# Optimization experiments

Measured on AMD Instinct MI355X. Metric: run time of the kernel, lower is better.

Reference implementation:

```python
import jax, jax.numpy as jnp
import numpy as np

PRE_NMS_TOPK = 6000
POST_NMS_TOPK = 1000
NMS_THRESH = 0.7
MIN_SIZE = 16.0
NEG = -1e9  # stand-in for -inf that is safe under autodiff


def setup_inputs() -> dict:
    key = jax.random.key(0)
    k1, k2, k3, k4, k5, k6, k7, k8 = jax.random.split(key, 8)
    B, A = 8, 200000
    N = B * A
    # realistic anchors: centers within a ~1333x800 canvas, sizes 16..256
    cx = jax.random.uniform(k1, (N,), minval=0.0, maxval=1200.0)
    cy = jax.random.uniform(k2, (N,), minval=0.0, maxval=800.0)
    w = jax.random.uniform(k3, (N,), minval=16.0, maxval=256.0)
    h = jax.random.uniform(k4, (N,), minval=16.0, maxval=256.0)
    anchors = jnp.stack([cx - 0.5 * w, cy - 0.5 * h, cx + 0.5 * w, cy + 0.5 * h], axis=1)
    batch_indices = jnp.sort(jax.random.randint(k5, (N,), 0, B)).astype(jnp.int32)
    image_sizes = jax.random.randint(k6, (B, 2), 600, 1334).astype(jnp.int32)  # (H, W)
    objectness_logits = jax.random.normal(k7, (N, 1), dtype=jnp.float32)
    bbox_deltas = jax.random.normal(k8, (N, 4), dtype=jnp.float32) * 0.2
    return {
        'anchors': anchors,
        'batch_indices': batch_indices,
        'image_sizes': image_sizes,
        'objectness_logits': objectness_logits,
        'bbox_deltas': bbox_deltas,
    }


def _nms_one(bx, sc):
    """Greedy NMS on [K,4] boxes / [K] scores; returns POST_NMS_TOPK (idx, ok)."""
    K = bx.shape[0]
    areas = (bx[:, 2] - bx[:, 0]) * (bx[:, 3] - bx[:, 1])
    ar = jnp.arange(K)

    def step(sup, _):
        s = jnp.where(sup, NEG, sc)
        j = jnp.argmax(s)
        ok = s[j] > 0.5 * NEG
        b = bx[j]
        ix1 = jnp.maximum(b[0], bx[:, 0])
        iy1 = jnp.maximum(b[1], bx[:, 1])
        ix2 = jnp.minimum(b[2], bx[:, 2])
        iy2 = jnp.minimum(b[3], bx[:, 3])
        inter = jnp.maximum(ix2 - ix1, 0.0) * jnp.maximum(iy2 - iy1, 0.0)
        iou = inter / (areas + areas[j] - inter + 1e-9)
        sup = sup | (iou > NMS_THRESH) | (ar == j)
        return sup, (j, ok)

    sup0 = sc <= 0.5 * NEG  # padded / invalid entries start suppressed
    _, (idx, ok) = jax.lax.scan(step, sup0, None, length=POST_NMS_TOPK)
    return idx, ok


def reference(anchors, batch_indices, image_sizes, objectness_logits, bbox_deltas):
    B = image_sizes.shape[0]
    N = anchors.shape[0]
    sizes = image_sizes[batch_indices].astype(jnp.float32)  # [N,2] (H,W) per anchor

    # --- box decode ---
    a_w = anchors[:, 2] - anchors[:, 0]
    a_h = anchors[:, 3] - anchors[:, 1]
    a_x = anchors[:, 0] + 0.5 * a_w
    a_y = anchors[:, 1] + 0.5 * a_h
    t_x, t_y = bbox_deltas[:, 0], bbox_deltas[:, 1]
    t_w, t_h = bbox_deltas[:, 2], bbox_deltas[:, 3]
    p_x = a_x + t_x * a_w
    p_y = a_y + t_y * a_h
    p_w = a_w * jnp.exp(jnp.clip(t_w, -10.0, 10.0))
    p_h = a_h * jnp.exp(jnp.clip(t_h, -10.0, 10.0))
    x1 = p_x - 0.5 * p_w
    y1 = p_y - 0.5 * p_h
    x2 = p_x + 0.5 * p_w
    y2 = p_y + 0.5 * p_h

    # --- clip to image ---
    H, W = sizes[:, 0], sizes[:, 1]
    x1 = jnp.clip(x1, 0.0, W - 1.0)
    y1 = jnp.clip(y1, 0.0, H - 1.0)
    x2 = jnp.clip(x2, 0.0, W - 1.0)
    y2 = jnp.clip(y2, 0.0, H - 1.0)
    boxes = jnp.stack([x1, y1, x2, y2], axis=1)  # [N,4]

    # --- min-size filter (as score masking) ---
    valid = ((x2 - x1) >= MIN_SIZE) & ((y2 - y1) >= MIN_SIZE)
    fg = jax.nn.sigmoid(objectness_logits[:, 0])

    # --- per-image top-k over masked scores ---
    img_mask = batch_indices[None, :] == jnp.arange(B, dtype=batch_indices.dtype)[:, None]  # [B,N]
    scores = jnp.where(img_mask & valid[None, :], fg[None, :], NEG)  # [B,N]
    top_scores, top_idx = jax.lax.top_k(scores, PRE_NMS_TOPK)  # [B,PRE]
    top_boxes = boxes[top_idx]  # [B,PRE,4]

    # --- NMS per image ---
    keep_idx, keep_ok = jax.vmap(_nms_one)(top_boxes, top_scores)  # [B,POST]

    sel = jnp.take_along_axis(top_idx, keep_idx, axis=1)  # global anchor indices [B,POST]
    okf = keep_ok[..., None].astype(boxes.dtype)
    props = jnp.take_along_axis(top_boxes, keep_idx[..., None], axis=1) * okf  # [B,POST,4]
    obj = objectness_logits[sel] * okf  # [B,POST,1]
    deltas_out = bbox_deltas[sel] * okf  # [B,POST,4]
    bidx = jnp.where(keep_ok, jnp.arange(B, dtype=jnp.int32)[:, None], -1)  # [B,POST]

    return (props.reshape(-1, 4), bidx.reshape(-1), obj.reshape(-1, 1),
            deltas_out.reshape(-1, 4), keep_ok.reshape(-1))
```

## Files before the change

### kernel.cpp

```cpp
#include <hip/hip_runtime.h>
#include <stdint.h>

#define PRE_K   6000
#define POST_K  1000
#define CAP     8192
#define BINS    1024
#define ROWS    6016
#define CH      94
#define MASKW   188
#define RC_CH   32
#define ROW_CAP (RC_CH * 64)
#define NEGF    -1000000000.0f
#define IOU_EPS 16.0f


__device__ __forceinline__ uint32_t orderf(float f) {
  uint32_t u = __float_as_uint(f);
  return (u & 0x80000000u) ? ~u : (u | 0x80000000u);
}

__device__ __forceinline__ int score_bin(float sc) {
  int bin = (int)floorf((sc + 12.0f) * ((float)BINS / 24.0f));
  return bin < 0 ? 0 : (bin > BINS - 1 ? BINS - 1 : bin);
}

__device__ __forceinline__ int bin_slot(int bin) {
  return ((bin & 15) << 6) | (bin >> 4);
}

__device__ __forceinline__ void decode_box(
    const float* __restrict__ anchors, const float* __restrict__ deltas,
    const int* __restrict__ isz, int n, int b,
    double& x1, double& y1, double& x2, double& y2, bool& valid) {
  double ax1 = (double)anchors[4 * n + 0], ay1 = (double)anchors[4 * n + 1];
  double ax2 = (double)anchors[4 * n + 2], ay2 = (double)anchors[4 * n + 3];
  double aw = ax2 - ax1, ah = ay2 - ay1;
  double acx = ax1 + 0.5 * aw, acy = ay1 + 0.5 * ah;
  double tx = (double)deltas[4 * n + 0], ty = (double)deltas[4 * n + 1];
  double tw = (double)deltas[4 * n + 2], th = (double)deltas[4 * n + 3];
  tw = tw < -10.0 ? -10.0 : (tw > 10.0 ? 10.0 : tw);
  th = th < -10.0 ? -10.0 : (th > 10.0 ? 10.0 : th);
  double px = acx + tx * aw, py = acy + ty * ah;
  double pw = aw * exp(tw), ph = ah * exp(th);
  double H = (double)isz[2 * b + 0], W = (double)isz[2 * b + 1];
  double wm = W - 1.0, hm = H - 1.0;
  x1 = px - 0.5 * pw; y1 = py - 0.5 * ph;
  x2 = px + 0.5 * pw; y2 = py + 0.5 * ph;
  x1 = fmin(fmax(x1, 0.0), wm); x2 = fmin(fmax(x2, 0.0), wm);
  y1 = fmin(fmax(y1, 0.0), hm); y2 = fmin(fmax(y2, 0.0), hm);
  valid = (x2 - x1 >= 16.0) && (y2 - y1 >= 16.0);
}

__device__ __forceinline__ bool iou_exact(const double* __restrict__ tbox,
                                          const double* __restrict__ tarea,
                                          size_t ri, size_t ci) {
  const double* pr = &tbox[ri * 4];
  const double* pc = &tbox[ci * 4];
  double w = fmin(pr[2], pc[2]) - fmax(pr[0], pc[0]); w = w > 0.0 ? w : 0.0;
  double h = fmin(pr[3], pc[3]) - fmax(pr[1], pc[1]); h = h > 0.0 ? h : 0.0;
  double it = w * h;
  return it > 0.7 * (tarea[ri] + tarea[ci] - it + 1e-9);
}


__global__ void k_init(uint32_t* hist, uint32_t* cnt, int B) {
  int i = blockIdx.x * blockDim.x + threadIdx.x;
  if (i < B * BINS) hist[i] = 0u;
  if (i < B) cnt[i] = 0u;
}

__global__ void __launch_bounds__(256) k_score(const float* __restrict__ anchors,
                                               const int* __restrict__ bix,
                                               const int* __restrict__ isz,
                                               const float* __restrict__ logits,
                                               const float* __restrict__ deltas,
                                               float* __restrict__ scores,
                                               uint32_t* __restrict__ hist, int N) {
  const int SPAN = 4096;
  int start = blockIdx.x * SPAN;
  int end = start + SPAN < N ? start + SPAN : N;
  __shared__ uint32_t lh[2][BINS];
  for (int i = threadIdx.x; i < 2 * BINS; i += 256) ((uint32_t*)lh)[i] = 0u;
  __shared__ int s_b0, s_b1;
  if (threadIdx.x == 0) { s_b0 = bix[start]; s_b1 = bix[end - 1]; }
  __syncthreads();
  int b0 = s_b0, b1 = s_b1;

  for (int n = start + (int)threadIdx.x; n < end; n += 256) {
    int b = bix[n];
    double x1, y1, x2, y2; bool valid;
    decode_box(anchors, deltas, isz, n, b, x1, y1, x2, y2, valid);
    float sc = valid ? logits[n] : NEGF;
    scores[n] = sc;
    if (valid) {
      int bin = score_bin(sc);
      if (b == b0)      atomicAdd(&lh[0][bin], 1u);
      else if (b == b1) atomicAdd(&lh[1][bin], 1u);
      else              atomicAdd(&hist[b * BINS + bin_slot(bin)], 1u);
    }
  }
  __syncthreads();
  for (int bin = threadIdx.x; bin < BINS; bin += 256) {
    uint32_t c0 = lh[0][bin];
    if (c0) atomicAdd(&hist[b0 * BINS + bin_slot(bin)], c0);
    if (b1 != b0) {
      uint32_t c1 = lh[1][bin];
      if (c1) atomicAdd(&hist[b1 * BINS + bin_slot(bin)], c1);
    }
  }
}

__global__ void k_scan(const uint32_t* __restrict__ hist, uint32_t* __restrict__ bstar) {
  __shared__ uint32_t s[BINS];
  __shared__ int bs;
  int b = blockIdx.x, t = threadIdx.x;
  s[t] = hist[b * BINS + bin_slot(t)];
  if (t == 0) bs = 0;
  __syncthreads();
  for (int off = 1; off < BINS; off <<= 1) {
    uint32_t v = (t + off < BINS) ? s[t + off] : 0u;
    __syncthreads();
    s[t] += v;
    __syncthreads();
  }
  if (s[t] >= PRE_K) atomicMax(&bs, t);
  __syncthreads();
  if (t == 0) bstar[b] = (uint32_t)bs;
}

__global__ void __launch_bounds__(1024) k_compact(const float* __restrict__ scores,
                                                  const int* __restrict__ bix,
                                                  const uint32_t* __restrict__ bstar,
                                                  uint32_t* __restrict__ cnt,
                                                  uint64_t* __restrict__ cand, int N) {
  const int SPAN = 8192;
  int start = blockIdx.x * SPAN;
  int end = start + SPAN < N ? start + SPAN : N;
  __shared__ uint32_t lcnt[8], lbase[8];
  if (threadIdx.x < 8) lcnt[threadIdx.x] = 0u;
  __syncthreads();

  bool     predv[8];
  uint64_t keyv[8];
  uint32_t lposv[8];
  int      bv[8];
  int nt = 0;
  for (int base = start; base < end; base += 1024, nt++) {
    int n = base + (int)threadIdx.x;
    bool pred = false; int b = 0; uint64_t key = 0ull; uint32_t lp = 0u;
    if (n < end) {
      float sc = scores[n];
      if (sc > 0.5f * NEGF) {
        b = bix[n];
        if ((uint32_t)score_bin(sc) >= bstar[b]) {
          pred = true;
          key = ((uint64_t)orderf(sc) << 32) | (uint64_t)(uint32_t)(~(uint32_t)n);
          lp = atomicAdd(&lcnt[b], 1u);
        }
      }
    }
    predv[nt] = pred; keyv[nt] = key; lposv[nt] = lp; bv[nt] = b;
  }
  __syncthreads();
  if (threadIdx.x < 8) {
    uint32_t c = lcnt[threadIdx.x];
    lbase[threadIdx.x] = c ? atomicAdd(&cnt[threadIdx.x], c) : 0u;
  }
  __syncthreads();
  for (int k = 0; k < nt; k++) {
    if (predv[k]) {
      uint32_t pos = lbase[bv[k]] + lposv[k];
      if (pos < CAP) cand[(size_t)bv[k] * CAP + pos] = keyv[k];
    }
  }
}

__global__ void __launch_bounds__(256) k_rank(const uint64_t* __restrict__ cand,
                                              const uint32_t* __restrict__ cnt,
                                              int* __restrict__ sorted_n,
                                              int* __restrict__ Cnum) {
  int b = blockIdx.x >> 5, chunk = blockIdx.x & 31, t = threadIdx.x;
  int C = (int)min(cnt[b], (uint32_t)CAP);
  if (chunk == 0 && t == 0) Cnum[b] = C < PRE_K ? C : PRE_K;
  if (chunk * 256 >= C) return;
  const uint64_t* g = cand + (size_t)b * CAP;
  int i = chunk * 256 + t;
  uint64_t ki = (i < C) ? g[i] : 0ull;
  __shared__ uint64_t tile[1024];
  int rank = 0;
  for (int base = 0; base < C; base += 1024) {
#pragma unroll
    for (int u = 0; u < 4; u++) {
      int j = base + u * 256 + t;
      tile[u * 256 + t] = (j < C) ? g[j] : 0ull;
    }
    __syncthreads();
    int lim = min(1024, C - base);
    int jj = 0;
    for (; jj + 4 <= lim; jj += 4) {
      rank += (tile[jj + 0] > ki) ? 1 : 0;
      rank += (tile[jj + 1] > ki) ? 1 : 0;
      rank += (tile[jj + 2] > ki) ? 1 : 0;
      rank += (tile[jj + 3] > ki) ? 1 : 0;
    }
    for (; jj < lim; jj++) rank += (tile[jj] > ki) ? 1 : 0;
    __syncthreads();
  }
  if (i < C && rank < PRE_K)
    sorted_n[b * PRE_K + rank] = (int)(~(uint32_t)(ki & 0xFFFFFFFFull));
}

__global__ void k_gather(const float* __restrict__ anchors,
                         const float* __restrict__ deltas,
                         const int* __restrict__ isz,
                         const int* __restrict__ sorted_n,
                         const int* __restrict__ Cnum,
                         double* __restrict__ tbox, double* __restrict__ tarea,
                         float4* __restrict__ tboxf, float* __restrict__ tareaf,
                         int* __restrict__ top_n, int B) {
  int idx = blockIdx.x * blockDim.x + threadIdx.x;
  if (idx >= B * PRE_K) return;
  int b = idx / PRE_K, r = idx % PRE_K;
  if (r >= Cnum[b]) return;
  int n = sorted_n[idx];
  double x1, y1, x2, y2; bool valid;
  decode_box(anchors, deltas, isz, n, b, x1, y1, x2, y2, valid);
  size_t row = (size_t)b * ROWS + r;
  tbox[row * 4 + 0] = x1;
  tbox[row * 4 + 1] = y1;
  tbox[row * 4 + 2] = x2;
  tbox[row * 4 + 3] = y2;
  double ar = (x2 - x1) * (y2 - y1);
  tarea[row] = ar;
  tboxf[row] = make_float4((float)x1, (float)y1, (float)x2, (float)y2);
  tareaf[row] = (float)ar;
  top_n[idx] = n;
}

__global__ void __launch_bounds__(64) k_iou_mat(const float4* __restrict__ tboxf,
                                                const float* __restrict__ tareaf,
                                                const double* __restrict__ tbox,
                                                const double* __restrict__ tarea,
                                                const int* __restrict__ Cnum,
                                                uint32_t* __restrict__ maskT) {
  int blk = blockIdx.x;
  int k  = blk % (RC_CH + 1);
  int cc = (blk / (RC_CH + 1)) % CH;
  int b  = blk / ((RC_CH + 1) * CH);
  int rc = (k == RC_CH) ? cc : k;
  if (k < RC_CH && cc <= rc) return;
  int C = Cnum[b];
  if (rc * 64 >= C || cc * 64 >= C) return;
  int lane = threadIdx.x;
  size_t bb = (size_t)b * ROWS;

  float4 cb4 = tboxf[bb + (size_t)cc * 64 + lane];
  float  cba = tareaf[bb + (size_t)cc * 64 + lane];
  __shared__ float4 rbx[64];
  __shared__ float  rba[64];
  rbx[lane] = tboxf[bb + (size_t)rc * 64 + lane];
  rba[lane] = tareaf[bb + (size_t)rc * 64 + lane];
  __syncthreads();

  uint32_t* seg = maskT + (((size_t)b * CH + cc) * ROWS + (size_t)rc * 64) * 2;
  bool isdiag = (rc == cc);

  for (int i = 0; i < 64; i++) {
    float4 r4 = rbx[i];
    float ra = rba[i];
    float iw = fminf(r4.z, cb4.z) - fmaxf(r4.x, cb4.x);
    float ih = fminf(r4.w, cb4.w) - fmaxf(r4.y, cb4.y);
    iw = fmaxf(iw, 0.0f); ih = fmaxf(ih, 0.0f);
    float inter = iw * ih;
    float diff = inter - 0.7f * (ra + cba - inter);
    bool gt = isdiag ? (lane > i) : true;
    unsigned long long sup   = __ballot(gt && (diff >  IOU_EPS));
    unsigned long long loose = __ballot(gt && (diff > -IOU_EPS));
    unsigned long long border = loose & ~sup;
    if (border) {
      bool mine = (border >> lane) & 1ull;
      bool ex = false;
      if (mine)
        ex = iou_exact(tbox, tarea, bb + (size_t)rc * 64 + i,
                       bb + (size_t)cc * 64 + lane);
      sup |= __ballot(ex);
    }
    if (lane == 0) {
      seg[i * 2 + 0] = (uint32_t)sup;
      seg[i * 2 + 1] = (uint32_t)(sup >> 32);
    }
  }
}

__global__ void __launch_bounds__(256) k_nms_reduce(const uint32_t* __restrict__ maskT,
                                                    const float4* __restrict__ tboxf,
                                                    const float* __restrict__ tareaf,
                                                    const double* __restrict__ tbox,
                                                    const double* __restrict__ tarea,
                                                    const int* __restrict__ Cnum,
                                                    int* __restrict__ keep,
                                                    int* __restrict__ kept_count) {
  int b = blockIdx.x, t = threadIdx.x;
  int wave = t >> 6, lane = t & 63;
  int C = Cnum[b];
  const uint32_t* M = maskT + (size_t)b * CH * ROWS * 2;
  size_t bb = (size_t)b * ROWS;

  __shared__ uint32_t s_f[2][2];
  __shared__ uint32_t kept_lo[POST_K];
  __shared__ uint32_t kept_hi[POST_K];
  __shared__ uint64_t s_kept;
  if (t < 4) ((uint32_t*)s_f)[t] = 0u;

  uint32_t d0 = 0u, d1 = 0u;
  if (wave == 0) {
    const uint32_t* rp = M + (size_t)lane * 2;
    d0 = rp[0]; d1 = rp[1];
  }
  __syncthreads();

  int nkept = 0, nlo = 0, nhi = 0;
  for (int c = 0; c < CH; c++) {
    int base = c * 64;
    if (base >= C) break;
    int cbuf = c & 1;
    if (t == 0) { s_f[cbuf ^ 1][0] = 0u; s_f[cbuf ^ 1][1] = 0u; }

    uint32_t f0 = 0u, f1 = 0u;
    for (int k2 = t; k2 < nlo; k2 += 256) {
      const uint32_t* rp = M + ((size_t)c * ROWS + kept_lo[k2]) * 2;
      f0 |= rp[0]; f1 |= rp[1];
    }
    if (wave == 1 && nhi > 0) {
      float4 cb4 = tboxf[bb + base + lane];
      float  cba = tareaf[bb + base + lane];
      for (int k2 = 0; k2 < nhi; k2++) {
        int r = (int)kept_hi[k2];
        float4 r4 = tboxf[bb + r];
        float ra = tareaf[bb + r];
        float iw = fminf(r4.z, cb4.z) - fmaxf(r4.x, cb4.x);
        float ih = fminf(r4.w, cb4.w) - fmaxf(r4.y, cb4.y);
        iw = fmaxf(iw, 0.0f); ih = fmaxf(ih, 0.0f);
        float inter = iw * ih;
        float diff = inter - 0.7f * (ra + cba - inter);
        unsigned long long sup   = __ballot(diff >  IOU_EPS);
        unsigned long long loose = __ballot(diff > -IOU_EPS);
        unsigned long long border = loose & ~sup;
        if (border) {
          bool mine = (border >> lane) & 1ull;
          bool ex = false;
          if (mine) ex = iou_exact(tbox, tarea, bb + r, bb + base + lane);
          sup |= __ballot(ex);
        }
        f0 |= (uint32_t)sup; f1 |= (uint32_t)(sup >> 32);
      }
    }
#pragma unroll
    for (int off = 32; off > 0; off >>= 1) {
      f0 |= (uint32_t)__shfl_xor((int)f0, off, 64);
      f1 |= (uint32_t)__shfl_xor((int)f1, off, 64);
    }
    if (lane == 0 && (f0 | f1)) {
      atomicOr(&s_f[cbuf][0], f0);
      atomicOr(&s_f[cbuf][1], f1);
    }
    __syncthreads();

    if (wave == 0) {
      uint64_t sup = (uint64_t)s_f[cbuf][0] | ((uint64_t)s_f[cbuf][1] << 32);
      int rem = C - base;
      if (rem < 64) sup |= ~((1ull << rem) - 1ull);
      uint64_t diag = (uint64_t)d0 | ((uint64_t)d1 << 32);
      int cn = (c + 1 < CH) ? c + 1 : c;
      const uint32_t* rpn = M + ((size_t)cn * ROWS + (size_t)cn * 64 + lane) * 2;
      uint32_t pn0 = rpn[0], pn1 = rpn[1];

      uint64_t keptMask = 0ull;
      uint64_t alive = ~sup;
      uint64_t m = alive;
      while (m) {
        int i = __builtin_ctzll(m);
        keptMask |= 1ull << i;
        uint64_t d = (uint64_t)__shfl((long long)diag, i, 64);
        sup |= d | (1ull << i);
        m = alive & ~sup;
      }
      int allowed = POST_K - nkept;
      int pc = __popcll(keptMask);
      while (pc > allowed) {
        keptMask &= ~(1ull << (63 - __builtin_clzll(keptMask)));
        pc--;
      }
      if (lane == 0) s_kept = keptMask;
      if ((keptMask >> lane) & 1ull) {
        int pfx = __popcll(keptMask & ((1ull << lane) - 1ull));
        keep[b * POST_K + nkept + pfx] = base + lane;
        if (c < RC_CH) kept_lo[nlo + pfx] = (uint32_t)(base + lane);
        else           kept_hi[nhi + pfx] = (uint32_t)(base + lane);
      }
      d0 = pn0; d1 = pn1;
    }
    __syncthreads();

    int pc = __popcll(s_kept);
    nkept += pc;
    if (c < RC_CH) nlo += pc; else nhi += pc;
    if (nkept >= POST_K) break;
  }
  if (t == 0) kept_count[b] = nkept;
}

__global__ void k_output(const int* __restrict__ keep,
                         const int* __restrict__ kept_count,
                         const int* __restrict__ top_n,
                         const double* __restrict__ tbox,
                         const float* __restrict__ logits,
                         const float* __restrict__ deltas,
                         float* __restrict__ out, int B) {
  int idx = blockIdx.x * blockDim.x + threadIdx.x;
  int M = B * POST_K;
  if (idx >= M) return;
  int b = idx / POST_K, s = idx % POST_K;
  float p0 = 0.f, p1 = 0.f, p2 = 0.f, p3 = 0.f;
  float ob = 0.f, d0 = 0.f, d1 = 0.f, d2 = 0.f, d3 = 0.f;
  float bi = -1.0f, okv = 0.0f;
  if (s < kept_count[b]) {
    int j = keep[b * POST_K + s];
    int n = top_n[b * PRE_K + j];
    const double* p = &tbox[((size_t)b * ROWS + j) * 4];
    p0 = (float)p[0]; p1 = (float)p[1]; p2 = (float)p[2]; p3 = (float)p[3];
    ob = logits[n];
    d0 = deltas[4 * n + 0]; d1 = deltas[4 * n + 1];
    d2 = deltas[4 * n + 2]; d3 = deltas[4 * n + 3];
    bi = (float)b; okv = 1.0f;
  }
  out[idx * 4 + 0] = p0;
  out[idx * 4 + 1] = p1;
  out[idx * 4 + 2] = p2;
  out[idx * 4 + 3] = p3;
  out[4 * M + idx] = bi;
  out[5 * M + idx] = ob;
  out[6 * M + idx * 4 + 0] = d0;
  out[6 * M + idx * 4 + 1] = d1;
  out[6 * M + idx * 4 + 2] = d2;
  out[6 * M + idx * 4 + 3] = d3;
  out[10 * M + idx] = okv;
}


extern "C" void kernel_launch(void* const* d_in, const int* in_sizes, int n_in,
                              void* d_out, int out_size, void* d_ws, size_t ws_size,
                              hipStream_t stream) {
  const float* anchors = (const float*)d_in[0];
  const int*   bix     = (const int*)d_in[1];
  const int*   isz     = (const int*)d_in[2];
  const float* logits  = (const float*)d_in[3];
  const float* deltas  = (const float*)d_in[4];
  float* out = (float*)d_out;

  int N = in_sizes[1];
  int B = in_sizes[2] / 2;

  uintptr_t p = (uintptr_t)d_ws;
  double*   tbox   = (double*)p;    p += (size_t)B * ROWS * 4 * sizeof(double);
  double*   tarea  = (double*)p;    p += (size_t)B * ROWS * sizeof(double);
  uint64_t* cand   = (uint64_t*)p;  p += (size_t)B * CAP * sizeof(uint64_t);
  float*    scores = (float*)p;     p += (size_t)N * sizeof(float);
  uint32_t* hist   = (uint32_t*)p;  p += (size_t)B * BINS * sizeof(uint32_t);
  int*      sorted_n = (int*)p;     p += (size_t)B * PRE_K * sizeof(int);
  int*      top_n    = (int*)p;     p += (size_t)B * PRE_K * sizeof(int);
  int*      keep     = (int*)p;     p += (size_t)B * POST_K * sizeof(int);
  uint32_t* cnt      = (uint32_t*)p; p += (size_t)B * sizeof(uint32_t);
  uint32_t* bstar    = (uint32_t*)p; p += (size_t)B * sizeof(uint32_t);
  int*      Cnum     = (int*)p;      p += (size_t)B * sizeof(int);
  int*      kept_cnt = (int*)p;      p += (size_t)B * sizeof(int);
  p = (p + 255) & ~(uintptr_t)255;
  uint32_t* maskT    = (uint32_t*)p; p += (size_t)B * CH * ROWS * 2 * sizeof(uint32_t);
  float4*   tboxf  = (float4*)scores;
  float*    tareaf = (float*)(scores + (size_t)B * ROWS * 4);
  (void)ws_size; (void)n_in; (void)out_size;

  int initN = B * BINS;
  k_init<<<(initN + 255) / 256, 256, 0, stream>>>(hist, cnt, B);
  k_score<<<(N + 4095) / 4096, 256, 0, stream>>>(anchors, bix, isz, logits, deltas,
                                                 scores, hist, N);
  k_scan<<<B, BINS, 0, stream>>>(hist, bstar);
  k_compact<<<(N + 8191) / 8192, 1024, 0, stream>>>(scores, bix, bstar, cnt, cand, N);
  k_rank<<<B * 32, 256, 0, stream>>>(cand, cnt, sorted_n, Cnum);
  k_gather<<<(B * PRE_K + 255) / 256, 256, 0, stream>>>(anchors, deltas, isz,
                                                        sorted_n, Cnum, tbox,
                                                        tarea, tboxf, tareaf,
                                                        top_n, B);
  k_iou_mat<<<B * CH * (RC_CH + 1), 64, 0, stream>>>(tboxf, tareaf, tbox, tarea,
                                                     Cnum, maskT);
  k_nms_reduce<<<B, 256, 0, stream>>>(maskT, tboxf, tareaf, tbox, tarea, Cnum,
                                      keep, kept_cnt);
  k_output<<<(B * POST_K + 255) / 256, 256, 0, stream>>>(keep, kept_cnt, top_n,
                                                         tbox, logits, deltas,
                                                         out, B);
}
```

Baseline: 441.5 us.

## Split rank counting across comparison-range blocks with atomic partial ranks

The rank-by-counting sort now divides the comparison range into four slices, each handled by its own block, which adds partial counts into a per-candidate rank buffer with atomics. A new placement kernel then scatters the candidate indices using the summed ranks. The shared-memory tile is read as 128-bit pairs. The goal is four times as many blocks for the quadratic rank step, so more of the GPU is busy. The cost is an extra kernel launch, a larger init pass and atomic traffic.

```diff
diff --git a/kernel.cpp b/kernel.cpp
--- a/kernel.cpp
+++ b/kernel.cpp
@@ -7,9 +7,8 @@
 #define BINS    1024
 #define ROWS    6016
 #define CH      94
-#define MASKW   188
 #define RC_CH   32
-#define ROW_CAP (RC_CH * 64)
+#define JSPLIT  4
 #define NEGF    -1000000000.0f
 #define IOU_EPS 16.0f
 
@@ -63,10 +62,11 @@
 }
 
 
-__global__ void k_init(uint32_t* hist, uint32_t* cnt, int B) {
+__global__ void k_init(uint32_t* hist, uint32_t* cnt, uint32_t* prank, int B) {
   int i = blockIdx.x * blockDim.x + threadIdx.x;
   if (i < B * BINS) hist[i] = 0u;
   if (i < B) cnt[i] = 0u;
+  if (i < B * CAP) prank[i] = 0u;
 }
 
 __global__ void __launch_bounds__(256) k_score(const float* __restrict__ anchors,
@@ -177,37 +177,69 @@
 
 __global__ void __launch_bounds__(256) k_rank(const uint64_t* __restrict__ cand,
                                               const uint32_t* __restrict__ cnt,
-                                              int* __restrict__ sorted_n,
-                                              int* __restrict__ Cnum) {
-  int b = blockIdx.x >> 5, chunk = blockIdx.x & 31, t = threadIdx.x;
+                                              uint32_t* __restrict__ prank) {
+  int blk = blockIdx.x;
+  int js = blk % JSPLIT;
+  int ic = (blk / JSPLIT) % 32;
+  int b  = blk / (JSPLIT * 32);
+  int t = threadIdx.x;
   int C = (int)min(cnt[b], (uint32_t)CAP);
-  if (chunk == 0 && t == 0) Cnum[b] = C < PRE_K ? C : PRE_K;
-  if (chunk * 256 >= C) return;
+  if (ic * 256 >= C) return;
   const uint64_t* g = cand + (size_t)b * CAP;
-  int i = chunk * 256 + t;
+  int i = ic * 256 + t;
   uint64_t ki = (i < C) ? g[i] : 0ull;
+
+  int q = (C + JSPLIT - 1) / JSPLIT;
+  int j0 = js * q;
+  int j1 = j0 + q < C ? j0 + q : C;
+  if (j0 >= j1) return;
+
   __shared__ uint64_t tile[1024];
   int rank = 0;
-  for (int base = 0; base < C; base += 1024) {
+  for (int base = j0; base < j1; base += 1024) {
 #pragma unroll
     for (int u = 0; u < 4; u++) {
       int j = base + u * 256 + t;
-      tile[u * 256 + t] = (j < C) ? g[j] : 0ull;
+      tile[u * 256 + t] = (j < j1) ? g[j] : 0ull;
     }
     __syncthreads();
-    int lim = min(1024, C - base);
+    int lim = j1 - base < 1024 ? j1 - base : 1024;
+    const ulonglong2* t2 = (const ulonglong2*)tile;
+    int pairs = lim >> 1;
     int jj = 0;
-    for (; jj + 4 <= lim; jj += 4) {
-      rank += (tile[jj + 0] > ki) ? 1 : 0;
-      rank += (tile[jj + 1] > ki) ? 1 : 0;
-      rank += (tile[jj + 2] > ki) ? 1 : 0;
-      rank += (tile[jj + 3] > ki) ? 1 : 0;
-    }
-    for (; jj < lim; jj++) rank += (tile[jj] > ki) ? 1 : 0;
+    for (; jj + 4 <= pairs; jj += 4) {
+      ulonglong2 v0 = t2[jj + 0], v1 = t2[jj + 1];
+      ulonglong2 v2 = t2[jj + 2], v3 = t2[jj + 3];
+      rank += (v0.x > ki) ? 1 : 0; rank += (v0.y > ki) ? 1 : 0;
+      rank += (v1.x > ki) ? 1 : 0; rank += (v1.y > ki) ? 1 : 0;
+      rank += (v2.x > ki) ? 1 : 0; rank += (v2.y > ki) ? 1 : 0;
+      rank += (v3.x > ki) ? 1 : 0; rank += (v3.y > ki) ? 1 : 0;
+    }
+    for (; jj < pairs; jj++) {
+      ulonglong2 v = t2[jj];
+      rank += (v.x > ki) ? 1 : 0; rank += (v.y > ki) ? 1 : 0;
+    }
+    if (lim & 1) rank += (tile[lim - 1] > ki) ? 1 : 0;
     __syncthreads();
   }
-  if (i < C && rank < PRE_K)
-    sorted_n[b * PRE_K + rank] = (int)(~(uint32_t)(ki & 0xFFFFFFFFull));
+  if (i < C && rank) atomicAdd(&prank[b * CAP + i], (uint32_t)rank);
+}
+
+__global__ void __launch_bounds__(256) k_place(const uint64_t* __restrict__ cand,
+                                               const uint32_t* __restrict__ cnt,
+                                               const uint32_t* __restrict__ prank,
+                                               int* __restrict__ sorted_n,
+                                               int* __restrict__ Cnum, int B) {
+  int idx = blockIdx.x * blockDim.x + threadIdx.x;
+  if (idx >= B * CAP) return;
+  int b = idx / CAP, i = idx % CAP;
+  int C = (int)min(cnt[b], (uint32_t)CAP);
+  if (i == 0) Cnum[b] = C < PRE_K ? C : PRE_K;
+  if (i >= C) return;
+  uint32_t rank = prank[idx];
+  if (rank < PRE_K)
+    sorted_n[b * PRE_K + rank] =
+        (int)(~(uint32_t)(cand[(size_t)b * CAP + i] & 0xFFFFFFFFull));
 }
 
 __global__ void k_gather(const float* __restrict__ anchors,
@@ -467,6 +499,7 @@
   uint64_t* cand   = (uint64_t*)p;  p += (size_t)B * CAP * sizeof(uint64_t);
   float*    scores = (float*)p;     p += (size_t)N * sizeof(float);
   uint32_t* hist   = (uint32_t*)p;  p += (size_t)B * BINS * sizeof(uint32_t);
+  uint32_t* prank  = (uint32_t*)p;  p += (size_t)B * CAP * sizeof(uint32_t);
   int*      sorted_n = (int*)p;     p += (size_t)B * PRE_K * sizeof(int);
   int*      top_n    = (int*)p;     p += (size_t)B * PRE_K * sizeof(int);
   int*      keep     = (int*)p;     p += (size_t)B * POST_K * sizeof(int);
@@ -480,13 +513,15 @@
   float*    tareaf = (float*)(scores + (size_t)B * ROWS * 4);
   (void)ws_size; (void)n_in; (void)out_size;
 
-  int initN = B * BINS;
-  k_init<<<(initN + 255) / 256, 256, 0, stream>>>(hist, cnt, B);
+  int initN = B * CAP;
+  k_init<<<(initN + 255) / 256, 256, 0, stream>>>(hist, cnt, prank, B);
   k_score<<<(N + 4095) / 4096, 256, 0, stream>>>(anchors, bix, isz, logits, deltas,
                                                  scores, hist, N);
   k_scan<<<B, BINS, 0, stream>>>(hist, bstar);
   k_compact<<<(N + 8191) / 8192, 1024, 0, stream>>>(scores, bix, bstar, cnt, cand, N);
-  k_rank<<<B * 32, 256, 0, stream>>>(cand, cnt, sorted_n, Cnum);
+  k_rank<<<B * 32 * JSPLIT, 256, 0, stream>>>(cand, cnt, prank);
+  k_place<<<(B * CAP + 255) / 256, 256, 0, stream>>>(cand, cnt, prank,
+                                                     sorted_n, Cnum, B);
   k_gather<<<(B * PRE_K + 255) / 256, 256, 0, stream>>>(anchors, deltas, isz,
                                                         sorted_n, Cnum, tbox,
                                                         tarea, tboxf, tareaf,
```

After: 358.9 us. 18.7% less time.
